# Kernel tuning notes

Hardware: AMD Instinct MI355X
Metric: run time of the kernel (lower is better)

Reference implementation:

```python
import jax, jax.numpy as jnp
import numpy as np

EMBED_DIM = 256
NUM_HEADS = 8


def setup_inputs() -> dict:
    key = jax.random.key(0)
    k1, k2, k3, k4 = jax.random.split(key, 4)
    b, nq, h, w = 2, 900, 16, 16
    attn_scores = jax.random.normal(k1, (b, nq, nq), dtype=jnp.float32)
    reference_points = jax.random.normal(k2, (b, nq, h, w), dtype=jnp.float32)
    # topology_proj = Linear(1, embed) -> ReLU -> Linear(embed, num_heads)
    w1 = jax.random.normal(k3, (EMBED_DIM,), dtype=jnp.float32) / 1.0  # Linear(1,E) weight, shape [E,1] squeezed
    b1 = jnp.zeros((EMBED_DIM,), dtype=jnp.float32)
    w2 = jax.random.normal(k4, (EMBED_DIM, NUM_HEADS), dtype=jnp.float32) / np.sqrt(EMBED_DIM)
    b2 = jnp.zeros((NUM_HEADS,), dtype=jnp.float32)
    lam = jnp.float32(0.1)
    return {"attn_scores": attn_scores, "reference_points": reference_points,
            "lam": lam, "w1": w1, "b1": b1, "w2": w2, "b2": b2}


def _process_reference_points(ref_pts):
    # ref_pts: [b, nq, h, w] -> argmax location normalized to [0,1]
    b, nq, h, w = ref_pts.shape
    flat = ref_pts.reshape(b, nq, h * w)
    idx = jnp.argmax(flat, axis=-1)                      # [b, nq] int
    y = (idx // w).astype(jnp.float32) / (h - 1)
    x = (idx % w).astype(jnp.float32) / (w - 1)
    return jnp.stack([x, y], axis=-1)                    # [b, nq, 2]


def reference(attn_scores, reference_points, lam, w1, b1, w2, b2):
    centers = _process_reference_points(reference_points)          # [b, nq, 2]
    # pairwise euclidean distance (torch.cdist)
    diff = centers[:, :, None, :] - centers[:, None, :, :]          # [b, nq, nq, 2]
    dist = jnp.sqrt(jnp.sum(diff * diff, axis=-1))                  # [b, nq, nq]
    mean_dist = jnp.mean(dist, axis=(1, 2), keepdims=True)
    topology = dist / (mean_dist + 1e-6)                            # [b, nq, nq]
    # tiny MLP on scalar feature: Linear(1,E) -> ReLU -> Linear(E,H)
    hdn = jax.nn.relu(topology[..., None] * w1 + b1)                # [b, nq, nq, E]
    bias = jnp.einsum('bqke,eh->bqkh', hdn, w2) + b2                # [b, nq, nq, H]
    bias_mean = jnp.mean(bias, axis=-1)                             # mean over heads -> [b, nq, nq]
    return attn_scores + lam * bias_mean
```

## Files before the change

### kernel.cpp

```cpp
#include <hip/hip_runtime.h>


#define NQ    900
#define LUT_N 451
#define TAG   0xC0DE0000u

__device__ __forceinline__ int aload_rlx(const int* p) {
    return __hip_atomic_load(p, __ATOMIC_RELAXED, __HIP_MEMORY_SCOPE_AGENT);
}
__device__ __forceinline__ void astore_rlx(int* p, int v) {
    __hip_atomic_store(p, v, __ATOMIC_RELAXED, __HIP_MEMORY_SCOPE_AGENT);
}

__global__ __launch_bounds__(256)
void k1_centers_stats(const float* __restrict__ ref,
                      const float* __restrict__ lam_p,
                      const float* __restrict__ w1,
                      const float* __restrict__ b1,
                      const float* __restrict__ w2,
                      const float* __restrict__ b2,
                      int* __restrict__ ws) {
    int*   cent2 = ws;
    float* lutp  = (float*)(ws + 900);
    int*   centp = ws + 900 + 2 * LUT_N;

    const int tid  = threadIdx.x;
    const int lane = tid & 63;
    const int wave = tid >> 6;
    const int blk  = blockIdx.x;

    if (blk < 450) {
        __shared__ int ctmp[4];
        int q = blk * 4 + wave;
        const float* p = ref + (size_t)q * 256;
        float bv = p[lane];
        int   bi = lane;
        #pragma unroll
        for (int k = 1; k < 4; ++k) {
            float v = p[lane + 64 * k];
            if (v > bv) { bv = v; bi = lane + 64 * k; }
        }
        #pragma unroll
        for (int off = 32; off >= 1; off >>= 1) {
            float ov = __shfl_down(bv, off, 64);
            int   oi = __shfl_down(bi, off, 64);
            if (ov > bv || (ov == bv && oi < bi)) { bv = ov; bi = oi; }
        }
        if (lane == 0) ctmp[wave] = bi;
        __syncthreads();
        if (tid == 0) {
            astore_rlx(&cent2[blk*2+0], (int)(TAG | ((ctmp[0]&255)<<8) | (ctmp[1]&255)));
            astore_rlx(&cent2[blk*2+1], (int)(TAG | ((ctmp[2]&255)<<8) | (ctmp[3]&255)));
        }
        return;
    }

    const int sb   = blk - 450;
    const int b    = sb >> 1;
    const int half = sb & 1;

    __shared__ int   idx_s[NQ];
    __shared__ float sqs[LUT_N];
    __shared__ int   hsh[256];
    __shared__ float w1s[256], b1s[256], wbars[256];
    __shared__ float wsum[4];

    hsh[tid] = 0;
    w1s[tid] = w1[tid];
    b1s[tid] = b1[tid];
    {
        float s8 = 0.f;
        #pragma unroll
        for (int h = 0; h < 8; ++h) s8 += w2[tid * 8 + h];
        wbars[tid] = s8 * 0.125f;
    }
    for (int s = tid; s < LUT_N; s += 256) sqs[s] = sqrtf((float)s);

    for (int k = tid; k < 450; k += 256) {
        int w;
        while (((unsigned)(w = aload_rlx(&cent2[b * 450 + k])) & 0xFFFF0000u) != TAG)
            __builtin_amdgcn_s_sleep(1);
        idx_s[2 * k]     = (w >> 8) & 255;
        idx_s[2 * k + 1] =  w       & 255;
    }
    __syncthreads();

    for (int k = tid; k < NQ; k += 256) atomicAdd(&hsh[idx_s[k]], 1);
    __syncthreads();

    float local = 0.f;
    {
        int h2v = hsh[tid];
        if (h2v) {
            int ix2 = tid & 15, iy2 = tid >> 4;
            for (int c1 = 0; c1 < 256; ++c1) {
                int h1 = hsh[c1];
                int dx = (c1 & 15) - ix2;
                int dy = (c1 >> 4) - iy2;
                local += (float)h1 * sqs[dx * dx + dy * dy];
            }
            local *= (float)h2v;
        }
    }
    #pragma unroll
    for (int off = 32; off >= 1; off >>= 1) local += __shfl_down(local, off, 64);
    if (lane == 0) wsum[wave] = local;
    __syncthreads();

    float tot   = wsum[0] + wsum[1] + wsum[2] + wsum[3];
    float mean  = tot * (1.f / 15.f) * (1.f / ((float)NQ * (float)NQ));
    float inv   = 1.f / (mean + 1e-6f);
    float b2bar = 0.125f * (b2[0] + b2[1] + b2[2] + b2[3] +
                            b2[4] + b2[5] + b2[6] + b2[7]);
    float lam   = lam_p[0];

    {
        int s0  = half * 226;
        int cnt = half ? 225 : 226;
        if (tid < cnt) {
            int   s   = s0 + tid;
            float t   = sqs[s] * (1.f / 15.f) * inv;
            float acc = b2bar;
            for (int i = 0; i < 256; ++i) {
                float hv = fmaf(t, w1s[i], b1s[i]);
                acc = fmaf(fmaxf(hv, 0.f), wbars[i], acc);
            }
            lutp[b * LUT_N + s] = lam * acc;
        }
    }
    if (half == 0 && tid < 225) {
        centp[b * 225 + tid] = (idx_s[4*tid] & 255) |
                               ((idx_s[4*tid+1] & 255) << 8) |
                               ((idx_s[4*tid+2] & 255) << 16) |
                               ((idx_s[4*tid+3] & 255) << 24);
    }
}

__global__ __launch_bounds__(256)
void k2_apply(const float* __restrict__ attn,
              const int* __restrict__ ws,
              float* __restrict__ out) {
    const float* lutp  = (const float*)(ws + 900);
    const int*   centp = ws + 900 + 2 * LUT_N;
    const int b = blockIdx.y;

    __shared__ float lut_s[LUT_N];
    __shared__ int   cpk[225];
    if (threadIdx.x < 225) cpk[threadIdx.x] = centp[b * 225 + threadIdx.x];
    for (int s = threadIdx.x; s < LUT_N; s += 256) lut_s[s] = lutp[b * LUT_N + s];
    __syncthreads();

    const int base_f4 = blockIdx.x * 1024 + threadIdx.x;
    #pragma unroll
    for (int u = 0; u < 4; ++u) {
        int f4 = base_f4 + u * 256;
        if (f4 < 202500) {
            int i  = f4 / 225;
            int j4 = f4 - i * 225;
            int ci = (cpk[i >> 2] >> ((i & 3) * 8)) & 255;
            int ixi = ci & 15, iyi = ci >> 4;
            int cw = cpk[j4];
            size_t g = (size_t)b * (NQ * NQ) + (size_t)i * NQ + j4 * 4;
            float4 a = *(const float4*)(attn + g);
            int c, dx, dy;
            c = cw & 255;         dx = ixi - (c & 15); dy = iyi - (c >> 4); a.x += lut_s[dx*dx + dy*dy];
            c = (cw >> 8) & 255;  dx = ixi - (c & 15); dy = iyi - (c >> 4); a.y += lut_s[dx*dx + dy*dy];
            c = (cw >> 16) & 255; dx = ixi - (c & 15); dy = iyi - (c >> 4); a.z += lut_s[dx*dx + dy*dy];
            c = (cw >> 24) & 255; dx = ixi - (c & 15); dy = iyi - (c >> 4); a.w += lut_s[dx*dx + dy*dy];
            *(float4*)(out + g) = a;
        }
    }
}

extern "C" void kernel_launch(void* const* d_in, const int* in_sizes, int n_in,
                              void* d_out, int out_size, void* d_ws, size_t ws_size,
                              hipStream_t stream) {
    const float* attn = (const float*)d_in[0];
    const float* ref  = (const float*)d_in[1];
    const float* lam  = (const float*)d_in[2];
    const float* w1   = (const float*)d_in[3];
    const float* b1   = (const float*)d_in[4];
    const float* w2   = (const float*)d_in[5];
    const float* b2   = (const float*)d_in[6];
    float* out = (float*)d_out;
    int*   ws  = (int*)d_ws;

    k1_centers_stats<<<454, 256, 0, stream>>>(ref, lam, w1, b1, w2, b2, ws);
    k2_apply<<<dim3(198, 2), 256, 0, stream>>>(attn, ws, out);
}
```

Baseline: 83.67 us.

## Recompute histogram and LUT per block and prefetch attn before stats

Kernel 1 now only computes argmax centers, using float4 loads, and drops the tagged spin-wait handoff. Kernel 2 has each block recompute the center histogram, mean distance and 451-entry LUT redundantly. Before that setup work, each block issues eight float4 loads of attn into registers so the memory traffic overlaps the setup compute. This removes the in-kernel spin synchronisation and the LUT round trip through global memory, but every one of the 198 blocks now repeats the O(256×256) histogram-distance pass and the LUT MLP, and holds more registers per thread.

Measured after the change: 85.56 us. 2.3% more time.

```diff
diff --git a/kernel.cpp b/kernel.cpp
--- a/kernel.cpp
+++ b/kernel.cpp
@@ -3,68 +3,71 @@
 
 #define NQ    900
 #define LUT_N 451
-#define TAG   0xC0DE0000u
 
-__device__ __forceinline__ int aload_rlx(const int* p) {
-    return __hip_atomic_load(p, __ATOMIC_RELAXED, __HIP_MEMORY_SCOPE_AGENT);
-}
-__device__ __forceinline__ void astore_rlx(int* p, int v) {
-    __hip_atomic_store(p, v, __ATOMIC_RELAXED, __HIP_MEMORY_SCOPE_AGENT);
+__global__ __launch_bounds__(256)
+void k1_centers(const float* __restrict__ ref, int* __restrict__ ws) {
+    __shared__ int ctmp[4];
+    const int tid  = threadIdx.x;
+    const int lane = tid & 63;
+    const int wave = tid >> 6;
+    const int q    = blockIdx.x * 4 + wave;
+
+    const float4* p4 = (const float4*)(ref + (size_t)q * 256);
+    float4 v = p4[lane];
+    float bv = v.x; int bi = lane * 4;
+    if (v.y > bv) { bv = v.y; bi = lane * 4 + 1; }
+    if (v.z > bv) { bv = v.z; bi = lane * 4 + 2; }
+    if (v.w > bv) { bv = v.w; bi = lane * 4 + 3; }
+    #pragma unroll
+    for (int off = 32; off >= 1; off >>= 1) {
+        float ov = __shfl_down(bv, off, 64);
+        int   oi = __shfl_down(bi, off, 64);
+        if (ov > bv || (ov == bv && oi < bi)) { bv = ov; bi = oi; }
+    }
+    if (lane == 0) ctmp[wave] = bi;
+    __syncthreads();
+    if (tid == 0)
+        ws[blockIdx.x] = (ctmp[0] & 255)        | ((ctmp[1] & 255) << 8) |
+                         ((ctmp[2] & 255) << 16) | ((ctmp[3] & 255) << 24);
 }
 
 __global__ __launch_bounds__(256)
-void k1_centers_stats(const float* __restrict__ ref,
-                      const float* __restrict__ lam_p,
-                      const float* __restrict__ w1,
-                      const float* __restrict__ b1,
-                      const float* __restrict__ w2,
-                      const float* __restrict__ b2,
-                      int* __restrict__ ws) {
-    int*   cent2 = ws;
-    float* lutp  = (float*)(ws + 900);
-    int*   centp = ws + 900 + 2 * LUT_N;
-
+void k2_stats_apply(const float* __restrict__ attn,
+                    const float* __restrict__ lam_p,
+                    const float* __restrict__ w1,
+                    const float* __restrict__ b1,
+                    const float* __restrict__ w2,
+                    const float* __restrict__ b2,
+                    const int* __restrict__ ws,
+                    float* __restrict__ out) {
     const int tid  = threadIdx.x;
     const int lane = tid & 63;
     const int wave = tid >> 6;
-    const int blk  = blockIdx.x;
+    const int b    = blockIdx.y;
 
-    if (blk < 450) {
-        __shared__ int ctmp[4];
-        int q = blk * 4 + wave;
-        const float* p = ref + (size_t)q * 256;
-        float bv = p[lane];
-        int   bi = lane;
+    const float4* attn4 = (const float4*)attn;
+    float4*       out4  = (float4*)out;
+    const int f4l = blockIdx.x * 2048 + tid;
+    float4 a[8];
+    if (blockIdx.x < 98) {
         #pragma unroll
-        for (int k = 1; k < 4; ++k) {
-            float v = p[lane + 64 * k];
-            if (v > bv) { bv = v; bi = lane + 64 * k; }
-        }
+        for (int u = 0; u < 8; ++u)
+            a[u] = attn4[(size_t)b * 202500 + f4l + u * 256];
+    } else {
         #pragma unroll
-        for (int off = 32; off >= 1; off >>= 1) {
-            float ov = __shfl_down(bv, off, 64);
-            int   oi = __shfl_down(bi, off, 64);
-            if (ov > bv || (ov == bv && oi < bi)) { bv = ov; bi = oi; }
-        }
-        if (lane == 0) ctmp[wave] = bi;
-        __syncthreads();
-        if (tid == 0) {
-            astore_rlx(&cent2[blk*2+0], (int)(TAG | ((ctmp[0]&255)<<8) | (ctmp[1]&255)));
-            astore_rlx(&cent2[blk*2+1], (int)(TAG | ((ctmp[2]&255)<<8) | (ctmp[3]&255)));
-        }
-        return;
+        for (int u = 0; u < 8; ++u)
+            if (f4l + u * 256 < 202500)
+                a[u] = attn4[(size_t)b * 202500 + f4l + u * 256];
     }
 
-    const int sb   = blk - 450;
-    const int b    = sb >> 1;
-    const int half = sb & 1;
-
-    __shared__ int   idx_s[NQ];
+    __shared__ int   cpk[225];
+    __shared__ int   hsh[256];
     __shared__ float sqs[LUT_N];
-    __shared__ int   hsh[256];
     __shared__ float w1s[256], b1s[256], wbars[256];
+    __shared__ float lut_s[LUT_N];
     __shared__ float wsum[4];
 
+    if (tid < 225) cpk[tid] = ws[b * 225 + tid];
     hsh[tid] = 0;
     w1s[tid] = w1[tid];
     b1s[tid] = b1[tid];
@@ -75,17 +78,12 @@
         wbars[tid] = s8 * 0.125f;
     }
     for (int s = tid; s < LUT_N; s += 256) sqs[s] = sqrtf((float)s);
-
-    for (int k = tid; k < 450; k += 256) {
-        int w;
-        while (((unsigned)(w = aload_rlx(&cent2[b * 450 + k])) & 0xFFFF0000u) != TAG)
-            __builtin_amdgcn_s_sleep(1);
-        idx_s[2 * k]     = (w >> 8) & 255;
-        idx_s[2 * k + 1] =  w       & 255;
-    }
     __syncthreads();
 
-    for (int k = tid; k < NQ; k += 256) atomicAdd(&hsh[idx_s[k]], 1);
+    for (int k = tid; k < NQ; k += 256) {
+        int c = (cpk[k >> 2] >> ((k & 3) * 8)) & 255;
+        atomicAdd(&hsh[c], 1);
+    }
     __syncthreads();
 
     float local = 0.f;
@@ -115,59 +113,40 @@
     float lam   = lam_p[0];
 
     {
-        int s0  = half * 226;
-        int cnt = half ? 225 : 226;
-        if (tid < cnt) {
-            int   s   = s0 + tid;
-            float t   = sqs[s] * (1.f / 15.f) * inv;
-            float acc = b2bar;
-            for (int i = 0; i < 256; ++i) {
-                float hv = fmaf(t, w1s[i], b1s[i]);
-                acc = fmaf(fmaxf(hv, 0.f), wbars[i], acc);
-            }
-            lutp[b * LUT_N + s] = lam * acc;
+        float t0   = sqs[tid] * (1.f / 15.f) * inv;
+        bool  has1 = (tid + 256 < LUT_N);
+        float t1   = has1 ? sqs[tid + 256] * (1.f / 15.f) * inv : 0.f;
+        float acc0 = b2bar, acc1 = b2bar;
+        for (int i = 0; i < 256; ++i) {
+            float w  = w1s[i];
+            float bb = b1s[i];
+            float wb = wbars[i];
+            float h0 = fmaf(t0, w, bb);
+            acc0 = fmaf(fmaxf(h0, 0.f), wb, acc0);
+            float h1 = fmaf(t1, w, bb);
+            acc1 = fmaf(fmaxf(h1, 0.f), wb, acc1);
         }
+        lut_s[tid] = lam * acc0;
+        if (has1) lut_s[tid + 256] = lam * acc1;
     }
-    if (half == 0 && tid < 225) {
-        centp[b * 225 + tid] = (idx_s[4*tid] & 255) |
-                               ((idx_s[4*tid+1] & 255) << 8) |
-                               ((idx_s[4*tid+2] & 255) << 16) |
-                               ((idx_s[4*tid+3] & 255) << 24);
-    }
-}
-
-__global__ __launch_bounds__(256)
-void k2_apply(const float* __restrict__ attn,
-              const int* __restrict__ ws,
-              float* __restrict__ out) {
-    const float* lutp  = (const float*)(ws + 900);
-    const int*   centp = ws + 900 + 2 * LUT_N;
-    const int b = blockIdx.y;
-
-    __shared__ float lut_s[LUT_N];
-    __shared__ int   cpk[225];
-    if (threadIdx.x < 225) cpk[threadIdx.x] = centp[b * 225 + threadIdx.x];
-    for (int s = threadIdx.x; s < LUT_N; s += 256) lut_s[s] = lutp[b * LUT_N + s];
     __syncthreads();
 
-    const int base_f4 = blockIdx.x * 1024 + threadIdx.x;
     #pragma unroll
-    for (int u = 0; u < 4; ++u) {
-        int f4 = base_f4 + u * 256;
+    for (int u = 0; u < 8; ++u) {
+        int f4 = f4l + u * 256;
         if (f4 < 202500) {
-            int i  = f4 / 225;
+            int i  = (int)((unsigned)f4 / 225u);
             int j4 = f4 - i * 225;
             int ci = (cpk[i >> 2] >> ((i & 3) * 8)) & 255;
             int ixi = ci & 15, iyi = ci >> 4;
             int cw = cpk[j4];
-            size_t g = (size_t)b * (NQ * NQ) + (size_t)i * NQ + j4 * 4;
-            float4 a = *(const float4*)(attn + g);
+            float4 v = a[u];
             int c, dx, dy;
-            c = cw & 255;         dx = ixi - (c & 15); dy = iyi - (c >> 4); a.x += lut_s[dx*dx + dy*dy];
-            c = (cw >> 8) & 255;  dx = ixi - (c & 15); dy = iyi - (c >> 4); a.y += lut_s[dx*dx + dy*dy];
-            c = (cw >> 16) & 255; dx = ixi - (c & 15); dy = iyi - (c >> 4); a.z += lut_s[dx*dx + dy*dy];
-            c = (cw >> 24) & 255; dx = ixi - (c & 15); dy = iyi - (c >> 4); a.w += lut_s[dx*dx + dy*dy];
-            *(float4*)(out + g) = a;
+            c = cw & 255;         dx = ixi - (c & 15); dy = iyi - (c >> 4); v.x += lut_s[dx*dx + dy*dy];
+            c = (cw >> 8) & 255;  dx = ixi - (c & 15); dy = iyi - (c >> 4); v.y += lut_s[dx*dx + dy*dy];
+            c = (cw >> 16) & 255; dx = ixi - (c & 15); dy = iyi - (c >> 4); v.z += lut_s[dx*dx + dy*dy];
+            c = (cw >> 24) & 255; dx = ixi - (c & 15); dy = iyi - (c >> 4); v.w += lut_s[dx*dx + dy*dy];
+            out4[(size_t)b * 202500 + f4] = v;
         }
     }
 }
@@ -185,6 +164,6 @@
     float* out = (float*)d_out;
     int*   ws  = (int*)d_ws;
 
-    k1_centers_stats<<<454, 256, 0, stream>>>(ref, lam, w1, b1, w2, b2, ws);
-    k2_apply<<<dim3(198, 2), 256, 0, stream>>>(attn, ws, out);
+    k1_centers<<<450, 256, 0, stream>>>(ref, ws);
+    k2_stats_apply<<<dim3(99, 2), 256, 0, stream>>>(attn, lam, w1, b1, w2, b2, ws, out);
 }
```
